# Performance work log

Hardware: AMD Instinct MI355X
Metric: run time of the kernel (lower is better)

Reference implementation:

```python
import jax, jax.numpy as jnp
import numpy as np

NUM_ITER = 3
SLOT_DIM = 16
INPUT_DIM = 256
HIDDEN_DIM = 128
EPS = 1e-8
LN_EPS = 1e-5  # torch LayerNorm default


def _layernorm(x, w, b):
    mu = jnp.mean(x, axis=-1, keepdims=True)
    var = jnp.mean((x - mu) ** 2, axis=-1, keepdims=True)
    return (x - mu) * jax.lax.rsqrt(var + LN_EPS) * w + b


def setup_inputs() -> dict:
    key = jax.random.key(0)
    ks = jax.random.split(key, 12)
    B, N, K = 32, 4096, 8
    D, S, H = INPUT_DIM, SLOT_DIM, HIDDEN_DIM
    inputs = jax.random.normal(ks[0], (B, N, D), dtype=jnp.float32)
    init_slots = jax.random.normal(ks[1], (B, K, S), dtype=jnp.float32)
    return {
        "inputs": inputs,
        "init_slots": init_slots,
        "ln_in_w": jnp.ones((D,), jnp.float32),
        "ln_in_b": jnp.zeros((D,), jnp.float32),
        "ln_s_w": jnp.ones((S,), jnp.float32),
        "ln_s_b": jnp.zeros((S,), jnp.float32),
        "ln_m_w": jnp.ones((S,), jnp.float32),
        "ln_m_b": jnp.zeros((S,), jnp.float32),
        "wq": jax.random.normal(ks[2], (S, S), jnp.float32) * (S ** -0.5),
        "wk": jax.random.normal(ks[3], (S, D), jnp.float32) * (D ** -0.5),
        "wv": jax.random.normal(ks[4], (S, D), jnp.float32) * (D ** -0.5),
        "w_ih": jax.random.normal(ks[5], (3 * S, S), jnp.float32) * (S ** -0.5),
        "w_hh": jax.random.normal(ks[6], (3 * S, S), jnp.float32) * (S ** -0.5),
        "b_ih": jnp.zeros((3 * S,), jnp.float32),
        "b_hh": jnp.zeros((3 * S,), jnp.float32),
        "mlp_w1": jax.random.normal(ks[7], (H, S), jnp.float32) * (S ** -0.5),
        "mlp_b1": jnp.zeros((H,), jnp.float32),
        "mlp_w2": jax.random.normal(ks[8], (S, H), jnp.float32) * (H ** -0.5),
        "mlp_b2": jnp.zeros((S,), jnp.float32),
    }


def _gru_cell(x, h, w_ih, w_hh, b_ih, b_hh):
    # torch GRUCell: gates ordered [r, z, n]
    gi = x @ w_ih.T + b_ih            # [BK, 3S]
    gh = h @ w_hh.T + b_hh
    i_r, i_z, i_n = jnp.split(gi, 3, axis=-1)
    h_r, h_z, h_n = jnp.split(gh, 3, axis=-1)
    r = jax.nn.sigmoid(i_r + h_r)
    z = jax.nn.sigmoid(i_z + h_z)
    n = jnp.tanh(i_n + r * h_n)
    return (1.0 - z) * n + z * h


def reference(inputs, init_slots, ln_in_w, ln_in_b, ln_s_w, ln_s_b, ln_m_w, ln_m_b,
              wq, wk, wv, w_ih, w_hh, b_ih, b_hh, mlp_w1, mlp_b1, mlp_w2, mlp_b2):
    B, N, _ = inputs.shape
    K = init_slots.shape[1]
    scale = SLOT_DIM ** -0.5

    x = _layernorm(inputs, ln_in_w, ln_in_b)
    k = jnp.einsum('bnd,sd->bns', x, wk)   # [B,N,S]
    v = jnp.einsum('bnd,sd->bns', x, wv)

    slots = init_slots
    attn = None
    for _ in range(NUM_ITER):
        slots_prev = slots
        q = jnp.einsum('bks,ts->bkt', _layernorm(slots, ln_s_w, ln_s_b), wq)
        logits = jnp.einsum('bks,bns->bkn', q, k) * scale       # [B,K,N]
        attn = jax.nn.softmax(logits, axis=1) + EPS              # softmax over SLOTS
        attn = attn / jnp.sum(attn, axis=-1, keepdims=True)
        updates = jnp.einsum('bkn,bns->bks', attn, v)            # [B,K,S]
        h = _gru_cell(updates.reshape(B * K, -1), slots_prev.reshape(B * K, -1),
                      w_ih, w_hh, b_ih, b_hh).reshape(B, K, -1)
        y = _layernorm(h, ln_m_w, ln_m_b)
        mlp = jax.nn.relu(y @ mlp_w1.T + mlp_b1) @ mlp_w2.T + mlp_b2
        slots = h + mlp
    return slots, attn
```

## Files before the change

### kernel.cpp

```cpp
#include <hip/hip_runtime.h>
#include <cstddef>


typedef unsigned short ushort_t;
typedef __attribute__((ext_vector_type(8))) short short8;
typedef __attribute__((ext_vector_type(4))) float f32x4;

__device__ __forceinline__ float sigmoid_f(float x){ return 1.f/(1.f+__expf(-x)); }
__device__ __forceinline__ float tanh_f(float x){ return 1.f - 2.f/(__expf(2.f*x)+1.f); }

__device__ __forceinline__ ushort_t f2bf(float x){
  unsigned u = __float_as_uint(x);
  return (ushort_t)((u + 0x7FFFu + ((u>>16)&1u)) >> 16);
}
__device__ __forceinline__ float bf2f(ushort_t b){
  return __uint_as_float(((unsigned)b) << 16);
}
__device__ __forceinline__ void split_bf(float v, short& hi, short& lo){
  unsigned u = __float_as_uint(v);
  hi = (short)(u >> 16);
  float hf = __uint_as_float(u & 0xFFFF0000u);
  lo = (short)(__float_as_uint(v - hf) >> 16);
}

__device__ __forceinline__ unsigned ld_cohpt(const unsigned* p){
  unsigned v;
  asm volatile("global_load_dword %0, %1, off sc0 sc1\n\t"
               "s_waitcnt vmcnt(0)"
               : "=v"(v) : "v"(p) : "memory");
  return v;
}

__global__ __launch_bounds__(256) void k_prep(
    const float* __restrict__ lnw, const float* __restrict__ lnb,
    const float* __restrict__ wk, const float* __restrict__ wv,
    const float* __restrict__ init_slots,
    const float* __restrict__ ln_s_w, const float* __restrict__ ln_s_b,
    const float* __restrict__ wq,
    ushort_t* __restrict__ Wh, ushort_t* __restrict__ Wl,
    float* __restrict__ mt,
    float* __restrict__ qbuf, float* __restrict__ upd, float* __restrict__ Abuf,
    unsigned* __restrict__ bar,
    float* __restrict__ slots_out)
{
  int t = threadIdx.x;
  int i = blockIdx.x*256 + t;
  {
    int s = i >> 8, d = i & 255;
    float w = (s < 16) ? wk[s*256+d] : wv[(s-16)*256+d];
    float w0 = lnw[d]*w;
    ushort_t hb = f2bf(w0);
    ushort_t lb = f2bf(w0 - bf2f(hb));
    Wh[i] = hb; Wl[i] = lb;
  }
  if (blockIdx.x != 0) return;
  {
    int s = t >> 3, j = t & 7;
    float m = 0.f, tv = 0.f;
    for (int d = j; d < 256; d += 8) {
      float w = (s < 16) ? wk[s*256+d] : wv[(s-16)*256+d];
      float w0 = lnw[d]*w;
      ushort_t hb = f2bf(w0);
      float hf = bf2f(hb);
      float lf = bf2f(f2bf(w0 - hf));
      m  += hf + lf;
      tv  = fmaf(lnb[d], w, tv);
    }
    m += __shfl_xor(m,1);  m += __shfl_xor(m,2);  m += __shfl_xor(m,4);
    tv += __shfl_xor(tv,1); tv += __shfl_xor(tv,2); tv += __shfl_xor(tv,4);
    if (j == 0) { mt[s] = m; mt[32+s] = tv; }
  }
  #pragma unroll
  for (int j2 = 0; j2 < 16; ++j2)
    slots_out[t*16+j2] = init_slots[t*16+j2];
  for (int i2 = t; i2 < 12288; i2 += 256) upd[i2] = 0.f;
  for (int i2 = t; i2 < 768;   i2 += 256) Abuf[i2] = 0.f;
  if (t < 96) bar[t] = 0u;
  float sl[16];
  #pragma unroll
  for (int j2 = 0; j2 < 16; ++j2) sl[j2] = init_slots[t*16+j2];
  float mu = 0.f;
  #pragma unroll
  for (int j2 = 0; j2 < 16; ++j2) mu += sl[j2];
  mu *= (1.f/16.f);
  float var = 0.f;
  #pragma unroll
  for (int j2 = 0; j2 < 16; ++j2) { float d = sl[j2]-mu; var = fmaf(d,d,var); }
  var *= (1.f/16.f);
  float rstd = rsqrtf(var + 1e-5f);
  float y[16];
  #pragma unroll
  for (int j2 = 0; j2 < 16; ++j2) y[j2] = (sl[j2]-mu)*rstd*ln_s_w[j2] + ln_s_b[j2];
  #pragma unroll
  for (int tq = 0; tq < 16; ++tq) {
    float q = 0.f;
    #pragma unroll
    for (int s2 = 0; s2 < 16; ++s2) q = fmaf(y[s2], wq[tq*16+s2], q);
    qbuf[t*16+tq] = q;
  }
}

#define VT_OFF    0
#define QS_OFF    16896
#define SLOTS_OFF 17408
#define APART_OFF 17920
#define X_OFF     18048
#define KLDS_OFF  (X_OFF + 33792)
#define PT_OFF    X_OFF
#define GW_OFF    (X_OFF + 8448)
#define SMEM_BYTES (X_OFF + 51200)

__global__ __launch_bounds__(256, 2) void k_mega(
    const float* __restrict__ x,
    const ushort_t* __restrict__ Wh, const ushort_t* __restrict__ Wl,
    const float* __restrict__ mt, const float* __restrict__ qbuf,
    const float* __restrict__ init_slots,
    float* __restrict__ upd, float* __restrict__ Abuf,
    unsigned* __restrict__ bar,
    float* __restrict__ slots_out, float* __restrict__ attn_out,
    const float* __restrict__ w_ih, const float* __restrict__ w_hh,
    const float* __restrict__ b_ih, const float* __restrict__ b_hh,
    const float* __restrict__ mlp_w1, const float* __restrict__ mlp_b1,
    const float* __restrict__ mlp_w2, const float* __restrict__ mlp_b2,
    const float* __restrict__ ln_m_w, const float* __restrict__ ln_m_b,
    const float* __restrict__ ln_s_w, const float* __restrict__ ln_s_b,
    const float* __restrict__ wq)
{
  __shared__ __align__(16) unsigned char smem[SMEM_BYTES];
  ushort_t* vt     = (ushort_t*)(smem + VT_OFF);
  float*    qs     = (float*)(smem + QS_OFF);
  float*    sslots = (float*)(smem + SLOTS_OFF);
  float*    apart  = (float*)(smem + APART_OFF);
  ushort_t* wlds   = (ushort_t*)(smem + X_OFF);
  float*    klds   = (float*)(smem + KLDS_OFF);
  ushort_t* pt     = (ushort_t*)(smem + PT_OFF);
  float*    s_wih  = (float*)(smem + GW_OFF);
  float*    s_whh  = s_wih + 48*17;
  float*    s_w1   = s_whh + 48*17;
  float*    s_w2   = s_w1 + 128*17;
  float*    s_bih  = s_w2 + 16*129;
  float*    s_bhh  = s_bih + 48;
  float*    s_b1   = s_bhh + 48;
  float*    s_b2   = s_b1 + 128;
  float*    s_lnmw = s_b2 + 16;
  float*    s_lnmb = s_lnmw + 16;
  float*    s_lnsw = s_lnmb + 16;
  float*    s_lnsb = s_lnsw + 16;
  float*    s_wq   = s_lnsb + 16;

  int t = threadIdx.x;
  int lane = t & 63;
  int w = t >> 6;
  int b  = blockIdx.x >> 4;
  int nc = blockIdx.x & 15;
  int n0 = nc << 8;

  {
    const unsigned* srcH = (const unsigned*)Wh;
    const unsigned* srcL = (const unsigned*)Wl;
    unsigned* dst = (unsigned*)wlds;
    #pragma unroll
    for (int i0 = 0; i0 < 8192; i0 += 256) {
      int i = i0 + t;
      int r = i >> 7, ww = i & 127;
      unsigned v = (r < 32) ? srcH[r*128 + ww] : srcL[(r-32)*128 + ww];
      dst[r*132 + ww] = v;
    }
  }
  __syncthreads();

  int m = lane & 15, quad = lane >> 4;
  const ushort_t* rhk = wlds + (size_t)m*264 + quad*8;
  const ushort_t* rhv = wlds + (size_t)(16+m)*264 + quad*8;
  const ushort_t* rlk = wlds + (size_t)(32+m)*264 + quad*8;
  const ushort_t* rlv = wlds + (size_t)(48+m)*264 + quad*8;
  float mtk  = mt[m],    mtv  = mt[16+m];
  float mtkb = mt[32+m], mtvb = mt[48+m];

  #pragma unroll
  for (int tile = 0; tile < 4; ++tile) {
    const float* xr = x + (size_t)(b*4096 + n0 + tile*64 + w*16 + m)*256 + quad*8;
    float4 xreg[16];
    #pragma unroll
    for (int kk = 0; kk < 8; ++kk) {
      xreg[2*kk]   = *(const float4*)(xr + kk*32);
      xreg[2*kk+1] = *(const float4*)(xr + kk*32 + 4);
    }
    f32x4 acck = {0.f,0.f,0.f,0.f}, accv = {0.f,0.f,0.f,0.f};
    float sum = 0.f, sumsq = 0.f;
    #pragma unroll
    for (int kk = 0; kk < 8; ++kk) {
      short8 bh_k = *(const short8*)(rhk + kk*32);
      short8 bh_v = *(const short8*)(rhv + kk*32);
      short8 bl_k = *(const short8*)(rlk + kk*32);
      short8 bl_v = *(const short8*)(rlv + kk*32);
      float xv[8] = {xreg[2*kk].x, xreg[2*kk].y, xreg[2*kk].z, xreg[2*kk].w,
                     xreg[2*kk+1].x, xreg[2*kk+1].y, xreg[2*kk+1].z, xreg[2*kk+1].w};
      short8 ah, al;
      #pragma unroll
      for (int j = 0; j < 8; ++j) {
        float v = xv[j];
        sum += v; sumsq = fmaf(v, v, sumsq);
        short h_, l_;
        split_bf(v, h_, l_);
        ah[j] = h_; al[j] = l_;
      }
      acck = __builtin_amdgcn_mfma_f32_16x16x32_bf16(ah, bh_k, acck, 0, 0, 0);
      accv = __builtin_amdgcn_mfma_f32_16x16x32_bf16(ah, bh_v, accv, 0, 0, 0);
      acck = __builtin_amdgcn_mfma_f32_16x16x32_bf16(al, bh_k, acck, 0, 0, 0);
      accv = __builtin_amdgcn_mfma_f32_16x16x32_bf16(al, bh_v, accv, 0, 0, 0);
      acck = __builtin_amdgcn_mfma_f32_16x16x32_bf16(ah, bl_k, acck, 0, 0, 0);
      accv = __builtin_amdgcn_mfma_f32_16x16x32_bf16(ah, bl_v, accv, 0, 0, 0);
    }
    sum   += __shfl_xor(sum, 16);   sum   += __shfl_xor(sum, 32);
    sumsq += __shfl_xor(sumsq, 16); sumsq += __shfl_xor(sumsq, 32);
    #pragma unroll
    for (int r = 0; r < 4; ++r) {
      int row = quad*4 + r;
      float s_ = __shfl(sum,   row);
      float q_ = __shfl(sumsq, row);
      float mu = s_*(1.f/256.f);
      float var = q_*(1.f/256.f) - mu*mu;
      float rstd = rsqrtf(var + 1e-5f);
      float ok = fmaf(rstd, acck[r] - mu*mtk, mtkb);
      float ov = fmaf(rstd, accv[r] - mu*mtv, mtvb);
      int gr = tile*64 + w*16 + row;
      klds[gr*17 + m] = ok;
      short h_, l_;
      split_bf(ov, h_, l_);
      vt[m*264 + gr]      = (ushort_t)h_;
      vt[(16+m)*264 + gr] = (ushort_t)l_;
    }
  }
  __syncthreads();
  float kv[16];
  #pragma unroll
  for (int j = 0; j < 16; ++j) kv[j] = klds[t*17 + j];
  __syncthreads();

  for (int i = t; i < 768; i += 256) {
    int g = i >> 4, j = i & 15;
    s_wih[g*17+j] = w_ih[i];
    s_whh[g*17+j] = w_hh[i];
  }
  for (int i = t; i < 2048; i += 256) {
    int r = i >> 4, c = i & 15;
    s_w1[r*17+c] = mlp_w1[i];
    int r2 = i >> 7, c2 = i & 127;
    s_w2[r2*129+c2] = mlp_w2[i];
  }
  if (t < 48) { s_bih[t] = b_ih[t]; s_bhh[t] = b_hh[t]; }
  if (t < 128) s_b1[t] = mlp_b1[t];
  if (t < 16) {
    s_b2[t] = mlp_b2[t];
    s_lnmw[t] = ln_m_w[t]; s_lnmb[t] = ln_m_b[t];
    s_lnsw[t] = ln_s_w[t]; s_lnsb[t] = ln_s_b[t];
  }
  for (int i = t; i < 256; i += 256) {
    int r = i >> 4, c = i & 15;
    s_wq[r*17+c] = wq[i];
  }
  if (t < 128) {
    qs[t]     = qbuf[b*128 + t];
    sslots[t] = init_slots[b*128 + t];
  }
  __syncthreads();

  const short8 z8 = {0,0,0,0,0,0,0,0};
  #pragma unroll 1
  for (int it = 0; it < 3; ++it) {
    float* upd_it = upd  + it*4096;
    float* Ab_it  = Abuf + it*256;

    float p8[8];
    {
      float lg[8];
      #pragma unroll
      for (int kk = 0; kk < 8; ++kk) {
        float a = 0.f;
        #pragma unroll
        for (int s = 0; s < 16; ++s) a = fmaf(qs[kk*16+s], kv[s], a);
        lg[kk] = a*0.25f;
      }
      float mx = lg[0];
      #pragma unroll
      for (int kk = 1; kk < 8; ++kk) mx = fmaxf(mx, lg[kk]);
      float se = 0.f;
      #pragma unroll
      for (int kk = 0; kk < 8; ++kk) { lg[kk] = __expf(lg[kk]-mx); se += lg[kk]; }
      float inv = 1.f/se;
      #pragma unroll
      for (int kk = 0; kk < 8; ++kk) p8[kk] = fmaf(lg[kk], inv, 1e-8f);
    }
    #pragma unroll
    for (int kk = 0; kk < 8; ++kk) {
      float r = p8[kk];
      r += __shfl_xor(r, 1);  r += __shfl_xor(r, 2);  r += __shfl_xor(r, 4);
      r += __shfl_xor(r, 8);  r += __shfl_xor(r, 16); r += __shfl_xor(r, 32);
      if (lane == 0) apart[w*8 + kk] = r;
    }
    #pragma unroll
    for (int kk = 0; kk < 8; ++kk) {
      short h_, l_;
      split_bf(p8[kk], h_, l_);
      pt[kk*264 + t]     = (ushort_t)h_;
      pt[(8+kk)*264 + t] = (ushort_t)l_;
    }
    __syncthreads();
    if (t < 8)
      atomicAdd(Ab_it + b*8 + t,
                apart[t] + apart[8+t] + apart[16+t] + apart[24+t]);
    if (w == 0) {
      int mm = lane & 15, q2 = lane >> 4;
      f32x4 acc = {0.f,0.f,0.f,0.f};
      #pragma unroll
      for (int c = 0; c < 8; ++c) {
        int k0 = c*32 + q2*8;
        short8 ah = (mm < 8) ? *(const short8*)&pt[mm*264 + k0]     : z8;
        short8 al = (mm < 8) ? *(const short8*)&pt[(8+mm)*264 + k0] : z8;
        short8 bh = *(const short8*)&vt[mm*264 + k0];
        short8 bl = *(const short8*)&vt[(16+mm)*264 + k0];
        acc = __builtin_amdgcn_mfma_f32_16x16x32_bf16(ah, bh, acc, 0, 0, 0);
        acc = __builtin_amdgcn_mfma_f32_16x16x32_bf16(al, bh, acc, 0, 0, 0);
        acc = __builtin_amdgcn_mfma_f32_16x16x32_bf16(ah, bl, acc, 0, 0, 0);
      }
      int s = lane & 15;
      #pragma unroll
      for (int r = 0; r < 4; ++r) {
        int kk = q2*4 + r;
        if (kk < 8) atomicAdd(upd_it + (b*8+kk)*16 + s, acc[r]);
      }
    }

    __syncthreads();
    if (t == 0) {
      unsigned* bp = bar + it*32 + b;
      asm volatile("s_waitcnt vmcnt(0)" ::: "memory");
      atomicAdd(bp, 1u);
      #pragma unroll 1
      for (int spin = 0; spin < (1<<18); ++spin) {
        if (ld_cohpt(bp) >= 16u) break;
        __builtin_amdgcn_s_sleep(2);
      }
    }
    __syncthreads();

    if (it == 2) {
      #pragma unroll
      for (int kk = 0; kk < 8; ++kk) {
        float Abk = __hip_atomic_load(Ab_it + b*8 + kk,
                                      __ATOMIC_RELAXED, __HIP_MEMORY_SCOPE_AGENT);
        attn_out[((size_t)(b*8 + kk))*4096 + n0 + t] = p8[kk]*(1.f/Abk);
      }
    }
    if (t < 128 && (it < 2 || nc == 0)) {
      int bk8 = t >> 4, s = t & 15;
      int laneBase = (t & 63) & ~15;
      float Ab = __hip_atomic_load(Ab_it + b*8 + bk8,
                                   __ATOMIC_RELAXED, __HIP_MEMORY_SCOPE_AGENT);
      float invA = 1.f / Ab;
      float u[16], h[16];
      #pragma unroll
      for (int j = 0; j < 16; ++j) {
        u[j] = __hip_atomic_load(upd_it + (b*8 + bk8)*16 + j,
                                 __ATOMIC_RELAXED, __HIP_MEMORY_SCOPE_AGENT) * invA;
        h[j] = sslots[bk8*16 + j];
      }
      float hs = h[s];
      float gir = s_bih[s],  giz = s_bih[16+s], gin = s_bih[32+s];
      float ghr = s_bhh[s],  ghz = s_bhh[16+s], ghn = s_bhh[32+s];
      #pragma unroll
      for (int j = 0; j < 16; ++j) {
        gir = fmaf(u[j], s_wih[s*17+j], gir);
        giz = fmaf(u[j], s_wih[(16+s)*17+j], giz);
        gin = fmaf(u[j], s_wih[(32+s)*17+j], gin);
        ghr = fmaf(h[j], s_whh[s*17+j], ghr);
        ghz = fmaf(h[j], s_whh[(16+s)*17+j], ghz);
        ghn = fmaf(h[j], s_whh[(32+s)*17+j], ghn);
      }
      float rr_ = sigmoid_f(gir + ghr);
      float zz = sigmoid_f(giz + ghz);
      float nn = tanh_f(gin + rr_*ghn);
      float hn = (1.f - zz)*nn + zz*hs;

      float ssum = hn;
      #pragma unroll
      for (int mm = 1; mm < 16; mm <<= 1) ssum += __shfl_xor(ssum, mm);
      float mu = ssum*(1.f/16.f);
      float dv = hn - mu;
      float vs = dv*dv;
      #pragma unroll
      for (int mm = 1; mm < 16; mm <<= 1) vs += __shfl_xor(vs, mm);
      float rstd = rsqrtf(vs*(1.f/16.f) + 1e-5f);
      float y = dv*rstd*s_lnmw[s] + s_lnmb[s];

      float yv[16];
      #pragma unroll
      for (int j = 0; j < 16; ++j) yv[j] = __shfl(y, laneBase + j);

      float h1[8];
      #pragma unroll
      for (int i = 0; i < 8; ++i) {
        int jj = i*16 + s;
        float a = s_b1[jj];
        #pragma unroll
        for (int q = 0; q < 16; ++q) a = fmaf(yv[q], s_w1[jj*17+q], a);
        h1[i] = fmaxf(a, 0.f);
      }
      float o = s_b2[s];
      #pragma unroll
      for (int i = 0; i < 8; ++i) {
        #pragma unroll
        for (int sp = 0; sp < 16; ++sp) {
          float hv = __shfl(h1[i], laneBase + sp);
          o = fmaf(hv, s_w2[s*129 + i*16 + sp], o);
        }
      }
      float slot_new = hn + o;
      if (it < 2) {
        sslots[bk8*16 + s] = slot_new;
        float ss = slot_new;
        #pragma unroll
        for (int mm = 1; mm < 16; mm <<= 1) ss += __shfl_xor(ss, mm);
        float mu2 = ss*(1.f/16.f);
        float d2 = slot_new - mu2;
        float v2 = d2*d2;
        #pragma unroll
        for (int mm = 1; mm < 16; mm <<= 1) v2 += __shfl_xor(v2, mm);
        float rstd2 = rsqrtf(v2*(1.f/16.f) + 1e-5f);
        float y2 = d2*rstd2*s_lnsw[s] + s_lnsb[s];
        float qv = 0.f;
        #pragma unroll
        for (int sp = 0; sp < 16; ++sp)
          qv = fmaf(__shfl(y2, laneBase + sp), s_wq[s*17+sp], qv);
        qs[bk8*16 + s] = qv;
      } else {
        slots_out[(b*8 + bk8)*16 + s] = slot_new;
      }
    }
    __syncthreads();
  }
}


__global__ __launch_bounds__(256, 4) void k_proj(
    const float* __restrict__ x, const ushort_t* __restrict__ Wh,
    const ushort_t* __restrict__ Wl, const float* __restrict__ mt,
    float* __restrict__ kout, float* __restrict__ vout)
{
  __shared__ ushort_t wlds[64*264];
  int t = threadIdx.x;
  int lane = t & 63;
  int p = __builtin_amdgcn_readfirstlane(t >> 6);
  int m = lane & 15, quad = lane >> 4;
  int r0 = blockIdx.x*64;
  {
    const unsigned* srcH = (const unsigned*)Wh;
    const unsigned* srcL = (const unsigned*)Wl;
    unsigned* dst = (unsigned*)wlds;
    #pragma unroll
    for (int i0 = 0; i0 < 8192; i0 += 256) {
      int i = i0 + t;
      int r = i >> 7, w = i & 127;
      unsigned v = (r < 32) ? srcH[r*128 + w] : srcL[(r-32)*128 + w];
      dst[r*132 + w] = v;
    }
  }
  __syncthreads();

  const ushort_t* rhk = wlds + (size_t)m*264 + quad*8;
  const ushort_t* rhv = wlds + (size_t)(16+m)*264 + quad*8;
  const ushort_t* rlk = wlds + (size_t)(32+m)*264 + quad*8;
  const ushort_t* rlv = wlds + (size_t)(48+m)*264 + quad*8;

  const float* xr = x + (size_t)(r0 + p*16 + m)*256 + quad*8;

  f32x4 acck = {0.f,0.f,0.f,0.f}, accv = {0.f,0.f,0.f,0.f};
  float sum = 0.f, sumsq = 0.f;

  #pragma unroll
  for (int kk = 0; kk < 8; ++kk) {
    float4 a0 = *(const float4*)(xr + kk*32);
    float4 a1 = *(const float4*)(xr + kk*32 + 4);
    short8 bh_k = *(const short8*)(rhk + kk*32);
    short8 bh_v = *(const short8*)(rhv + kk*32);
    short8 bl_k = *(const short8*)(rlk + kk*32);
    short8 bl_v = *(const short8*)(rlv + kk*32);
    float xv[8] = {a0.x,a0.y,a0.z,a0.w, a1.x,a1.y,a1.z,a1.w};
    short8 ah, al;
    #pragma unroll
    for (int j = 0; j < 8; ++j) {
      float v = xv[j];
      sum += v; sumsq = fmaf(v, v, sumsq);
      short h_, l_;
      split_bf(v, h_, l_);
      ah[j] = h_; al[j] = l_;
    }
    acck = __builtin_amdgcn_mfma_f32_16x16x32_bf16(ah, bh_k, acck, 0, 0, 0);
    accv = __builtin_amdgcn_mfma_f32_16x16x32_bf16(ah, bh_v, accv, 0, 0, 0);
    acck = __builtin_amdgcn_mfma_f32_16x16x32_bf16(al, bh_k, acck, 0, 0, 0);
    accv = __builtin_amdgcn_mfma_f32_16x16x32_bf16(al, bh_v, accv, 0, 0, 0);
    acck = __builtin_amdgcn_mfma_f32_16x16x32_bf16(ah, bl_k, acck, 0, 0, 0);
    accv = __builtin_amdgcn_mfma_f32_16x16x32_bf16(ah, bl_v, accv, 0, 0, 0);
  }

  sum   += __shfl_xor(sum, 16);  sum   += __shfl_xor(sum, 32);
  sumsq += __shfl_xor(sumsq, 16); sumsq += __shfl_xor(sumsq, 32);

  float mtk  = mt[m],    mtv  = mt[16+m];
  float mtkb = mt[32+m], mtvb = mt[48+m];
  #pragma unroll
  for (int r = 0; r < 4; ++r) {
    int row = quad*4 + r;
    float s_ = __shfl(sum,   row);
    float q_ = __shfl(sumsq, row);
    float mu = s_*(1.f/256.f);
    float var = q_*(1.f/256.f) - mu*mu;
    float rstd = rsqrtf(var + 1e-5f);
    float ok = fmaf(rstd, acck[r] - mu*mtk, mtkb);
    float ov = fmaf(rstd, accv[r] - mu*mtv, mtvb);
    size_t grow = (size_t)(r0 + p*16 + row)*16 + m;
    kout[grow] = ok;
    vout[grow] = ov;
  }
}

__global__ __launch_bounds__(256) void k_attn(
    const float* __restrict__ kproj, const float* __restrict__ vproj,
    const float* __restrict__ qbuf,
    float* __restrict__ upd, float* __restrict__ Abuf,
    float* __restrict__ attn_out, int write_attn)
{
  __shared__ ushort_t vt[32*264];
  __shared__ ushort_t pt[32*264];
  __shared__ float qs[128];
  __shared__ float apart[4][8];
  int b = blockIdx.x >> 4;
  int n0 = (blockIdx.x & 15) * 256;
  int t = threadIdx.x;
  int w = t >> 6, lane = t & 63;

  if (t < 128) qs[t] = qbuf[b*128 + t];

  const float* kr = kproj + ((size_t)(b*4096 + n0 + t))*16;
  const float* vr = vproj + ((size_t)(b*4096 + n0 + t))*16;
  float kv[16], vv[16];
  #pragma unroll
  for (int j = 0; j < 16; j += 4) {
    float4 f = *(const float4*)(kr+j);
    kv[j]=f.x; kv[j+1]=f.y; kv[j+2]=f.z; kv[j+3]=f.w;
    float4 g = *(const float4*)(vr+j);
    vv[j]=g.x; vv[j+1]=g.y; vv[j+2]=g.z; vv[j+3]=g.w;
  }
  #pragma unroll
  for (int s = 0; s < 16; ++s) {
    short h_, l_;
    split_bf(vv[s], h_, l_);
    vt[s*264 + t] = (ushort_t)h_;
    vt[(16+s)*264 + t] = (ushort_t)l_;
  }
  __syncthreads();

  float p8[8];
  {
    float lg[8];
    #pragma unroll
    for (int kk = 0; kk < 8; ++kk) {
      float a = 0.f;
      #pragma unroll
      for (int s = 0; s < 16; ++s) a = fmaf(qs[kk*16+s], kv[s], a);
      lg[kk] = a*0.25f;
    }
    float mx = lg[0];
    #pragma unroll
    for (int kk = 1; kk < 8; ++kk) mx = fmaxf(mx, lg[kk]);
    float se = 0.f;
    #pragma unroll
    for (int kk = 0; kk < 8; ++kk) { lg[kk] = __expf(lg[kk]-mx); se += lg[kk]; }
    float inv = 1.f/se;
    #pragma unroll
    for (int kk = 0; kk < 8; ++kk) {
      float pv = fmaf(lg[kk], inv, 1e-8f);
      p8[kk] = pv;
      if (write_attn) attn_out[((size_t)(b*8+kk))*4096 + n0 + t] = pv;
    }
  }
  #pragma unroll
  for (int kk = 0; kk < 8; ++kk) {
    float r = p8[kk];
    r += __shfl_xor(r, 1);  r += __shfl_xor(r, 2);  r += __shfl_xor(r, 4);
    r += __shfl_xor(r, 8);  r += __shfl_xor(r, 16); r += __shfl_xor(r, 32);
    if (lane == 0) apart[w][kk] = r;
  }
  #pragma unroll
  for (int kk = 0; kk < 8; ++kk) {
    short h_, l_;
    split_bf(p8[kk], h_, l_);
    pt[kk*264 + t] = (ushort_t)h_;
    pt[(16+kk)*264 + t] = (ushort_t)l_;
  }
  __syncthreads();

  if (t < 8)
    atomicAdd(Abuf + b*8 + t,
              apart[0][t] + apart[1][t] + apart[2][t] + apart[3][t]);

  if (w == 0) {
    int mm = lane & 15, quad = lane >> 4;
    const short8 z8 = {0,0,0,0,0,0,0,0};
    f32x4 acc = {0.f,0.f,0.f,0.f};
    #pragma unroll
    for (int c = 0; c < 8; ++c) {
      int k0 = c*32 + quad*8;
      short8 ah = (mm < 8) ? *(const short8*)&pt[mm*264 + k0]      : z8;
      short8 al = (mm < 8) ? *(const short8*)&pt[(16+mm)*264 + k0] : z8;
      short8 bh = *(const short8*)&vt[mm*264 + k0];
      short8 bl = *(const short8*)&vt[(16+mm)*264 + k0];
      acc = __builtin_amdgcn_mfma_f32_16x16x32_bf16(ah, bh, acc, 0, 0, 0);
      acc = __builtin_amdgcn_mfma_f32_16x16x32_bf16(al, bh, acc, 0, 0, 0);
      acc = __builtin_amdgcn_mfma_f32_16x16x32_bf16(ah, bl, acc, 0, 0, 0);
    }
    int s = lane & 15;
    #pragma unroll
    for (int r = 0; r < 4; ++r) {
      int kk = quad*4 + r;
      if (kk < 8) atomicAdd(upd + (b*8+kk)*16 + s, acc[r]);
    }
  }
}

__device__ __forceinline__ void gru_body(
    int bk, int s, int laneBase, int prep_next,
    float* upd, float* Abuf, float* slots, float* qbuf,
    const float* s_wih, const float* s_whh,
    const float* s_bih, const float* s_bhh,
    const float* s_w1, const float* s_b1,
    const float* s_w2, const float* s_b2,
    const float* s_lnmw, const float* s_lnmb,
    const float* s_lnsw, const float* s_lnsb, const float* s_wq)
{
  float inv = 1.f / Abuf[bk];
  float u[16], h[16];
  #pragma unroll
  for (int j = 0; j < 16; ++j) {
    u[j] = upd[bk*16+j] * inv;
    h[j] = slots[bk*16+j];
  }
  float hs = slots[bk*16+s];

  float gir = s_bih[s],  giz = s_bih[16+s], gin = s_bih[32+s];
  float ghr = s_bhh[s],  ghz = s_bhh[16+s], ghn = s_bhh[32+s];
  #pragma unroll
  for (int j = 0; j < 16; ++j) {
    gir = fmaf(u[j], s_wih[s*17+j], gir);
    giz = fmaf(u[j], s_wih[(16+s)*17+j], giz);
    gin = fmaf(u[j], s_wih[(32+s)*17+j], gin);
    ghr = fmaf(h[j], s_whh[s*17+j], ghr);
    ghz = fmaf(h[j], s_whh[(16+s)*17+j], ghz);
    ghn = fmaf(h[j], s_whh[(32+s)*17+j], ghn);
  }
  float rr = sigmoid_f(gir + ghr);
  float zz = sigmoid_f(giz + ghz);
  float nn = tanh_f(gin + rr*ghn);
  float hn = (1.f-zz)*nn + zz*hs;

  float ssum = hn;
  #pragma unroll
  for (int mm = 1; mm < 16; mm <<= 1) ssum += __shfl_xor(ssum, mm);
  float mu = ssum*(1.f/16.f);
  float dv = hn - mu;
  float vs = dv*dv;
  #pragma unroll
  for (int mm = 1; mm < 16; mm <<= 1) vs += __shfl_xor(vs, mm);
  float rstd = rsqrtf(vs*(1.f/16.f) + 1e-5f);
  float y = dv*rstd*s_lnmw[s] + s_lnmb[s];

  float yv[16];
  #pragma unroll
  for (int j = 0; j < 16; ++j) yv[j] = __shfl(y, laneBase + j);

  float h1[8];
  #pragma unroll
  for (int i = 0; i < 8; ++i) {
    int jj = i*16 + s;
    float a = s_b1[jj];
    #pragma unroll
    for (int q = 0; q < 16; ++q) a = fmaf(yv[q], s_w1[jj*17+q], a);
    h1[i] = fmaxf(a, 0.f);
  }
  float o = s_b2[s];
  #pragma unroll
  for (int i = 0; i < 8; ++i) {
    #pragma unroll
    for (int sp = 0; sp < 16; ++sp) {
      float hv = __shfl(h1[i], laneBase + sp);
      o = fmaf(hv, s_w2[s*129 + i*16 + sp], o);
    }
  }
  float slot_new = hn + o;
  slots[bk*16+s] = slot_new;

  if (prep_next) {
    float ss = slot_new;
    #pragma unroll
    for (int mm = 1; mm < 16; mm <<= 1) ss += __shfl_xor(ss, mm);
    float mu2 = ss*(1.f/16.f);
    float d2 = slot_new - mu2;
    float v2 = d2*d2;
    #pragma unroll
    for (int mm = 1; mm < 16; mm <<= 1) v2 += __shfl_xor(v2, mm);
    float rstd2 = rsqrtf(v2*(1.f/16.f) + 1e-5f);
    float y2 = d2*rstd2*s_lnsw[s] + s_lnsb[s];
    float qv = 0.f;
    #pragma unroll
    for (int sp = 0; sp < 16; ++sp)
      qv = fmaf(__shfl(y2, laneBase+sp), s_wq[s*17+sp], qv);
    qbuf[bk*16+s] = qv;
    upd[bk*16+s] = 0.f;
    if (s == 0) Abuf[bk] = 0.f;
  }
}

#define GRU_STAGE_LDS()                                                      \
  __shared__ float s_wih[48*17], s_whh[48*17];                               \
  __shared__ float s_bih[48], s_bhh[48];                                     \
  __shared__ float s_w1[128*17], s_b1[128];                                  \
  __shared__ float s_w2[16*129], s_b2[16];                                   \
  __shared__ float s_lnmw[16], s_lnmb[16], s_lnsw[16], s_lnsb[16];           \
  __shared__ float s_wq[16*17];                                              \
  {                                                                          \
    int t_ = threadIdx.x;                                                    \
    for (int i = t_; i < 768; i += 256) {                                    \
      int g = i >> 4, j = i & 15;                                            \
      s_wih[g*17+j] = w_ih[i];                                               \
      s_whh[g*17+j] = w_hh[i];                                               \
    }                                                                        \
    for (int i = t_; i < 2048; i += 256) {                                   \
      int r = i >> 4, c = i & 15;                                            \
      s_w1[r*17+c] = mlp_w1[i];                                              \
      int r2 = i >> 7, c2 = i & 127;                                         \
      s_w2[r2*129+c2] = mlp_w2[i];                                           \
    }                                                                        \
    if (t_ < 48) { s_bih[t_] = b_ih[t_]; s_bhh[t_] = b_hh[t_]; }             \
    if (t_ < 128) s_b1[t_] = mlp_b1[t_];                                     \
    if (t_ < 16) {                                                           \
      s_b2[t_] = mlp_b2[t_];                                                 \
      s_lnmw[t_] = ln_m_w[t_]; s_lnmb[t_] = ln_m_b[t_];                      \
      s_lnsw[t_] = ln_s_w[t_]; s_lnsb[t_] = ln_s_b[t_];                      \
    }                                                                        \
    for (int i = t_; i < 256; i += 256) {                                    \
      int r = i >> 4, c = i & 15;                                            \
      s_wq[r*17+c] = wq[i];                                                  \
    }                                                                        \
  }                                                                          \
  __syncthreads();

__global__ __launch_bounds__(256) void k_gru(
    float* __restrict__ upd, float* __restrict__ Abuf,
    float* __restrict__ slots, float* __restrict__ qbuf,
    const float* __restrict__ w_ih, const float* __restrict__ w_hh,
    const float* __restrict__ b_ih, const float* __restrict__ b_hh,
    const float* __restrict__ mlp_w1, const float* __restrict__ mlp_b1,
    const float* __restrict__ mlp_w2, const float* __restrict__ mlp_b2,
    const float* __restrict__ ln_m_w, const float* __restrict__ ln_m_b,
    const float* __restrict__ ln_s_w, const float* __restrict__ ln_s_b,
    const float* __restrict__ wq)
{
  GRU_STAGE_LDS()
  int t = threadIdx.x;
  int bk = blockIdx.x*16 + (t >> 4);
  int s = t & 15;
  int laneBase = (t & 63) & ~15;
  gru_body(bk, s, laneBase, 1, upd, Abuf, slots, qbuf,
           s_wih, s_whh, s_bih, s_bhh, s_w1, s_b1, s_w2, s_b2,
           s_lnmw, s_lnmb, s_lnsw, s_lnsb, s_wq);
}

__global__ __launch_bounds__(256) void k_final(
    float* __restrict__ upd, float* __restrict__ Abuf,
    float* __restrict__ slots, float* __restrict__ qbuf,
    float* __restrict__ attn,
    const float* __restrict__ w_ih, const float* __restrict__ w_hh,
    const float* __restrict__ b_ih, const float* __restrict__ b_hh,
    const float* __restrict__ mlp_w1, const float* __restrict__ mlp_b1,
    const float* __restrict__ mlp_w2, const float* __restrict__ mlp_b2,
    const float* __restrict__ ln_m_w, const float* __restrict__ ln_m_b,
    const float* __restrict__ ln_s_w, const float* __restrict__ ln_s_b,
    const float* __restrict__ wq)
{
  int t = threadIdx.x;
  {
    int bk = blockIdx.x;
    float inv = 1.f / Abuf[bk];
    float4* p = (float4*)(attn + (size_t)bk*4096);
    #pragma unroll 4
    for (int i = t; i < 1024; i += 256) {
      float4 v = p[i];
      v.x *= inv; v.y *= inv; v.z *= inv; v.w *= inv;
      p[i] = v;
    }
  }
  if (blockIdx.x >= 16) return;
  GRU_STAGE_LDS()
  int bk = blockIdx.x*16 + (t >> 4);
  int s = t & 15;
  int laneBase = (t & 63) & ~15;
  gru_body(bk, s, laneBase, 0, upd, Abuf, slots, qbuf,
           s_wih, s_whh, s_bih, s_bhh, s_w1, s_b1, s_w2, s_b2,
           s_lnmw, s_lnmb, s_lnsw, s_lnsb, s_wq);
}

extern "C" void kernel_launch(void* const* d_in, const int* in_sizes, int n_in,
                              void* d_out, int out_size, void* d_ws, size_t ws_size,
                              hipStream_t stream)
{
  const float* inputs     = (const float*)d_in[0];
  const float* init_slots = (const float*)d_in[1];
  const float* ln_in_w    = (const float*)d_in[2];
  const float* ln_in_b    = (const float*)d_in[3];
  const float* ln_s_w     = (const float*)d_in[4];
  const float* ln_s_b     = (const float*)d_in[5];
  const float* ln_m_w     = (const float*)d_in[6];
  const float* ln_m_b     = (const float*)d_in[7];
  const float* wq         = (const float*)d_in[8];
  const float* wk         = (const float*)d_in[9];
  const float* wv         = (const float*)d_in[10];
  const float* w_ih       = (const float*)d_in[11];
  const float* w_hh       = (const float*)d_in[12];
  const float* b_ih       = (const float*)d_in[13];
  const float* b_hh       = (const float*)d_in[14];
  const float* mlp_w1     = (const float*)d_in[15];
  const float* mlp_b1     = (const float*)d_in[16];
  const float* mlp_w2     = (const float*)d_in[17];
  const float* mlp_b2     = (const float*)d_in[18];

  float* ws    = (float*)d_ws;
  ushort_t* Wh = (ushort_t*)ws;
  ushort_t* Wl = (ushort_t*)(ws + 4096);
  float* mt    = ws + 8192;
  float* qbuf  = ws + 8320;
  float* upd   = ws + 12416;
  float* Abuf  = ws + 24704;
  unsigned* bar = (unsigned*)(ws + 25472);
  float* kproj = ws + 25600;
  float* vproj = kproj + 2097152;

  float* out   = (float*)d_out;
  float* slots = out;
  float* attn  = out + 4096;

  static int s_mode = -1;
  if (s_mode < 0) {
    int dev = 0;
    (void)hipGetDevice(&dev);
    int ncu = 0;
    (void)hipDeviceGetAttribute(&ncu, hipDeviceAttributeMultiprocessorCount, dev);
    int nb = 0;
    if (hipOccupancyMaxActiveBlocksPerMultiprocessor(&nb, (const void*)k_mega,
                                                     256, 0) != hipSuccess)
      nb = 0;
    s_mode = (nb > 0 && ncu > 0 && (long)nb * ncu >= 512) ? 0 : 1;
  }

  k_prep<<<32, 256, 0, stream>>>(ln_in_w, ln_in_b, wk, wv, init_slots,
                                 ln_s_w, ln_s_b, wq,
                                 Wh, Wl, mt, qbuf, upd, Abuf, bar, slots);

  if (s_mode == 0) {
    k_mega<<<512, 256, 0, stream>>>(inputs, Wh, Wl, mt, qbuf, init_slots,
                                    upd, Abuf, bar, slots, attn,
                                    w_ih, w_hh, b_ih, b_hh,
                                    mlp_w1, mlp_b1, mlp_w2, mlp_b2,
                                    ln_m_w, ln_m_b, ln_s_w, ln_s_b, wq);
    return;
  }

  {
    void* kargs[] = {
      (void*)&inputs, (void*)&Wh, (void*)&Wl, (void*)&mt, (void*)&qbuf,
      (void*)&init_slots, (void*)&upd, (void*)&Abuf, (void*)&bar,
      (void*)&slots, (void*)&attn, (void*)&w_ih, (void*)&w_hh,
      (void*)&b_ih, (void*)&b_hh, (void*)&mlp_w1, (void*)&mlp_b1,
      (void*)&mlp_w2, (void*)&mlp_b2, (void*)&ln_m_w, (void*)&ln_m_b,
      (void*)&ln_s_w, (void*)&ln_s_b, (void*)&wq };
    hipError_t err = hipLaunchCooperativeKernel((const void*)k_mega,
                                                dim3(512), dim3(256),
                                                kargs, 0, stream);
    if (err == hipSuccess) return;
    (void)hipGetLastError();
  }

  k_proj<<<2048, 256, 0, stream>>>(inputs, Wh, Wl, mt, kproj, vproj);
  for (int it = 0; it < 3; ++it) {
    int last = (it == 2);
    k_attn<<<512, 256, 0, stream>>>(kproj, vproj, qbuf, upd, Abuf, attn, last);
    if (!last)
      k_gru<<<16, 256, 0, stream>>>(upd, Abuf, slots, qbuf,
                                    w_ih, w_hh, b_ih, b_hh,
                                    mlp_w1, mlp_b1, mlp_w2, mlp_b2,
                                    ln_m_w, ln_m_b, ln_s_w, ln_s_b, wq);
  }
  k_final<<<256, 256, 0, stream>>>(upd, Abuf, slots, qbuf, attn,
                                   w_ih, w_hh, b_ih, b_hh,
                                   mlp_w1, mlp_b1, mlp_w2, mlp_b2,
                                   ln_m_w, ln_m_b, ln_s_w, ln_s_b, wq);
}
```

Before: 335.5 us.

## Fold prep into mega kernel and replace atomics with per-chunk partial buffers

```diff
diff --git a/kernel.cpp b/kernel.cpp
--- a/kernel.cpp
+++ b/kernel.cpp
@@ -30,81 +30,20 @@
                : "=v"(v) : "v"(p) : "memory");
   return v;
 }
-
-__global__ __launch_bounds__(256) void k_prep(
-    const float* __restrict__ lnw, const float* __restrict__ lnb,
-    const float* __restrict__ wk, const float* __restrict__ wv,
-    const float* __restrict__ init_slots,
-    const float* __restrict__ ln_s_w, const float* __restrict__ ln_s_b,
-    const float* __restrict__ wq,
-    ushort_t* __restrict__ Wh, ushort_t* __restrict__ Wl,
-    float* __restrict__ mt,
-    float* __restrict__ qbuf, float* __restrict__ upd, float* __restrict__ Abuf,
-    unsigned* __restrict__ bar,
-    float* __restrict__ slots_out)
-{
-  int t = threadIdx.x;
-  int i = blockIdx.x*256 + t;
-  {
-    int s = i >> 8, d = i & 255;
-    float w = (s < 16) ? wk[s*256+d] : wv[(s-16)*256+d];
-    float w0 = lnw[d]*w;
-    ushort_t hb = f2bf(w0);
-    ushort_t lb = f2bf(w0 - bf2f(hb));
-    Wh[i] = hb; Wl[i] = lb;
-  }
-  if (blockIdx.x != 0) return;
-  {
-    int s = t >> 3, j = t & 7;
-    float m = 0.f, tv = 0.f;
-    for (int d = j; d < 256; d += 8) {
-      float w = (s < 16) ? wk[s*256+d] : wv[(s-16)*256+d];
-      float w0 = lnw[d]*w;
-      ushort_t hb = f2bf(w0);
-      float hf = bf2f(hb);
-      float lf = bf2f(f2bf(w0 - hf));
-      m  += hf + lf;
-      tv  = fmaf(lnb[d], w, tv);
-    }
-    m += __shfl_xor(m,1);  m += __shfl_xor(m,2);  m += __shfl_xor(m,4);
-    tv += __shfl_xor(tv,1); tv += __shfl_xor(tv,2); tv += __shfl_xor(tv,4);
-    if (j == 0) { mt[s] = m; mt[32+s] = tv; }
-  }
-  #pragma unroll
-  for (int j2 = 0; j2 < 16; ++j2)
-    slots_out[t*16+j2] = init_slots[t*16+j2];
-  for (int i2 = t; i2 < 12288; i2 += 256) upd[i2] = 0.f;
-  for (int i2 = t; i2 < 768;   i2 += 256) Abuf[i2] = 0.f;
-  if (t < 96) bar[t] = 0u;
-  float sl[16];
-  #pragma unroll
-  for (int j2 = 0; j2 < 16; ++j2) sl[j2] = init_slots[t*16+j2];
-  float mu = 0.f;
-  #pragma unroll
-  for (int j2 = 0; j2 < 16; ++j2) mu += sl[j2];
-  mu *= (1.f/16.f);
-  float var = 0.f;
-  #pragma unroll
-  for (int j2 = 0; j2 < 16; ++j2) { float d = sl[j2]-mu; var = fmaf(d,d,var); }
-  var *= (1.f/16.f);
-  float rstd = rsqrtf(var + 1e-5f);
-  float y[16];
-  #pragma unroll
-  for (int j2 = 0; j2 < 16; ++j2) y[j2] = (sl[j2]-mu)*rstd*ln_s_w[j2] + ln_s_b[j2];
-  #pragma unroll
-  for (int tq = 0; tq < 16; ++tq) {
-    float q = 0.f;
-    #pragma unroll
-    for (int s2 = 0; s2 < 16; ++s2) q = fmaf(y[s2], wq[tq*16+s2], q);
-    qbuf[t*16+tq] = q;
-  }
+__device__ __forceinline__ void st_agent(float* p, float v){
+  __hip_atomic_store(p, v, __ATOMIC_RELAXED, __HIP_MEMORY_SCOPE_AGENT);
+}
+__device__ __forceinline__ float ld_agent(const float* p){
+  return __hip_atomic_load(p, __ATOMIC_RELAXED, __HIP_MEMORY_SCOPE_AGENT);
 }
 
 #define VT_OFF    0
 #define QS_OFF    16896
 #define SLOTS_OFF 17408
 #define APART_OFF 17920
-#define X_OFF     18048
+#define ULDS_OFF  18048
+#define MT_OFF    18560
+#define X_OFF     18816
 #define KLDS_OFF  (X_OFF + 33792)
 #define PT_OFF    X_OFF
 #define GW_OFF    (X_OFF + 8448)
@@ -112,11 +51,11 @@
 
 __global__ __launch_bounds__(256, 2) void k_mega(
     const float* __restrict__ x,
-    const ushort_t* __restrict__ Wh, const ushort_t* __restrict__ Wl,
-    const float* __restrict__ mt, const float* __restrict__ qbuf,
+    const float* __restrict__ wk, const float* __restrict__ wv,
+    const float* __restrict__ lnw, const float* __restrict__ lnb,
     const float* __restrict__ init_slots,
-    float* __restrict__ upd, float* __restrict__ Abuf,
-    unsigned* __restrict__ bar,
+    float* __restrict__ updp, float* __restrict__ Asum,
+    unsigned* __restrict__ barp,
     float* __restrict__ slots_out, float* __restrict__ attn_out,
     const float* __restrict__ w_ih, const float* __restrict__ w_hh,
     const float* __restrict__ b_ih, const float* __restrict__ b_hh,
@@ -131,6 +70,8 @@
   float*    qs     = (float*)(smem + QS_OFF);
   float*    sslots = (float*)(smem + SLOTS_OFF);
   float*    apart  = (float*)(smem + APART_OFF);
+  float*    ulds   = (float*)(smem + ULDS_OFF);
+  float*    mtf    = (float*)(smem + MT_OFF);
   ushort_t* wlds   = (ushort_t*)(smem + X_OFF);
   float*    klds   = (float*)(smem + KLDS_OFF);
   ushort_t* pt     = (ushort_t*)(smem + PT_OFF);
@@ -156,17 +97,69 @@
   int n0 = nc << 8;
 
   {
-    const unsigned* srcH = (const unsigned*)Wh;
-    const unsigned* srcL = (const unsigned*)Wl;
     unsigned* dst = (unsigned*)wlds;
     #pragma unroll
     for (int i0 = 0; i0 < 8192; i0 += 256) {
       int i = i0 + t;
       int r = i >> 7, ww = i & 127;
-      unsigned v = (r < 32) ? srcH[r*128 + ww] : srcL[(r-32)*128 + ww];
-      dst[r*132 + ww] = v;
-    }
-  }
+      int s = (r & 31);
+      int d = ww*2;
+      float wa = (s < 16) ? wk[s*256+d]   : wv[(s-16)*256+d];
+      float wb = (s < 16) ? wk[s*256+d+1] : wv[(s-16)*256+d+1];
+      float w0a = lnw[d]*wa, w0b = lnw[d+1]*wb;
+      ushort_t ha = f2bf(w0a), hb2 = f2bf(w0b);
+      unsigned word;
+      if (r < 32) {
+        word = (unsigned)ha | ((unsigned)hb2 << 16);
+      } else {
+        ushort_t la = f2bf(w0a - bf2f(ha));
+        ushort_t lb = f2bf(w0b - bf2f(hb2));
+        word = (unsigned)la | ((unsigned)lb << 16);
+      }
+      dst[r*132 + ww] = word;
+    }
+  }
+  {
+    int s = t >> 3, j = t & 7;
+    float m = 0.f, tv = 0.f;
+    for (int d = j; d < 256; d += 8) {
+      float w_ = (s < 16) ? wk[s*256+d] : wv[(s-16)*256+d];
+      float w0 = lnw[d]*w_;
+      ushort_t hb = f2bf(w0);
+      float hf = bf2f(hb);
+      float lf = bf2f(f2bf(w0 - hf));
+      m  += hf + lf;
+      tv  = fmaf(lnb[d], w_, tv);
+    }
+    m += __shfl_xor(m,1);  m += __shfl_xor(m,2);  m += __shfl_xor(m,4);
+    tv += __shfl_xor(tv,1); tv += __shfl_xor(tv,2); tv += __shfl_xor(tv,4);
+    if (j == 0) { mtf[s] = m; mtf[32+s] = tv; }
+  }
+  if (t < 8) {
+    float sl[16];
+    #pragma unroll
+    for (int j2 = 0; j2 < 16; ++j2) sl[j2] = init_slots[(b*8+t)*16+j2];
+    float mu = 0.f;
+    #pragma unroll
+    for (int j2 = 0; j2 < 16; ++j2) mu += sl[j2];
+    mu *= (1.f/16.f);
+    float var = 0.f;
+    #pragma unroll
+    for (int j2 = 0; j2 < 16; ++j2) { float d = sl[j2]-mu; var = fmaf(d,d,var); }
+    var *= (1.f/16.f);
+    float rstd = rsqrtf(var + 1e-5f);
+    float y[16];
+    #pragma unroll
+    for (int j2 = 0; j2 < 16; ++j2) y[j2] = (sl[j2]-mu)*rstd*ln_s_w[j2] + ln_s_b[j2];
+    #pragma unroll
+    for (int tq = 0; tq < 16; ++tq) {
+      float q = 0.f;
+      #pragma unroll
+      for (int s2 = 0; s2 < 16; ++s2) q = fmaf(y[s2], wq[tq*16+s2], q);
+      qs[t*16+tq] = q;
+    }
+  }
+  if (t < 128) sslots[t] = init_slots[b*128 + t];
   __syncthreads();
 
   int m = lane & 15, quad = lane >> 4;
@@ -174,8 +167,8 @@
   const ushort_t* rhv = wlds + (size_t)(16+m)*264 + quad*8;
   const ushort_t* rlk = wlds + (size_t)(32+m)*264 + quad*8;
   const ushort_t* rlv = wlds + (size_t)(48+m)*264 + quad*8;
-  float mtk  = mt[m],    mtv  = mt[16+m];
-  float mtkb = mt[32+m], mtvb = mt[48+m];
+  float mtk  = mtf[m],    mtv  = mtf[16+m];
+  float mtkb = mtf[32+m], mtvb = mtf[48+m];
 
   #pragma unroll
   for (int tile = 0; tile < 4; ++tile) {
@@ -260,17 +253,13 @@
     int r = i >> 4, c = i & 15;
     s_wq[r*17+c] = wq[i];
   }
-  if (t < 128) {
-    qs[t]     = qbuf[b*128 + t];
-    sslots[t] = init_slots[b*128 + t];
-  }
   __syncthreads();
 
   const short8 z8 = {0,0,0,0,0,0,0,0};
   #pragma unroll 1
   for (int it = 0; it < 3; ++it) {
-    float* upd_it = upd  + it*4096;
-    float* Ab_it  = Abuf + it*256;
+    float* upd_it = updp + (size_t)(it*32 + b)*2048;
+    float* As_it  = Asum + (size_t)(it*32 + b)*128;
 
     float p8[8];
     {
@@ -308,8 +297,8 @@
     }
     __syncthreads();
     if (t < 8)
-      atomicAdd(Ab_it + b*8 + t,
-                apart[t] + apart[8+t] + apart[16+t] + apart[24+t]);
+      st_agent(As_it + nc*8 + t,
+               apart[t] + apart[8+t] + apart[16+t] + apart[24+t]);
     if (w == 0) {
       int mm = lane & 15, q2 = lane >> 4;
       f32x4 acc = {0.f,0.f,0.f,0.f};
@@ -328,42 +317,52 @@
       #pragma unroll
       for (int r = 0; r < 4; ++r) {
         int kk = q2*4 + r;
-        if (kk < 8) atomicAdd(upd_it + (b*8+kk)*16 + s, acc[r]);
+        if (kk < 8) st_agent(upd_it + nc*128 + kk*16 + s, acc[r]);
       }
     }
 
     __syncthreads();
     if (t == 0) {
-      unsigned* bp = bar + it*32 + b;
+      unsigned* bp = barp + (it*32 + b)*32;
       asm volatile("s_waitcnt vmcnt(0)" ::: "memory");
       atomicAdd(bp, 1u);
       #pragma unroll 1
       for (int spin = 0; spin < (1<<18); ++spin) {
         if (ld_cohpt(bp) >= 16u) break;
-        __builtin_amdgcn_s_sleep(2);
+        __builtin_amdgcn_s_sleep(8);
       }
     }
     __syncthreads();
 
+    if (t < 8) {
+      float a = 0.f;
+      #pragma unroll
+      for (int nc2 = 0; nc2 < 16; ++nc2) a += ld_agent(As_it + nc2*8 + t);
+      apart[t] = a;
+    }
+    if (t < 128) {
+      int bk8 = t >> 4, s = t & 15;
+      float us = 0.f;
+      #pragma unroll
+      for (int nc2 = 0; nc2 < 16; ++nc2)
+        us += ld_agent(upd_it + nc2*128 + bk8*16 + s);
+      ulds[t] = us;
+    }
+    __syncthreads();
+
     if (it == 2) {
       #pragma unroll
-      for (int kk = 0; kk < 8; ++kk) {
-        float Abk = __hip_atomic_load(Ab_it + b*8 + kk,
-                                      __ATOMIC_RELAXED, __HIP_MEMORY_SCOPE_AGENT);
-        attn_out[((size_t)(b*8 + kk))*4096 + n0 + t] = p8[kk]*(1.f/Abk);
-      }
+      for (int kk = 0; kk < 8; ++kk)
+        attn_out[((size_t)(b*8 + kk))*4096 + n0 + t] = p8[kk]*(1.f/apart[kk]);
     }
     if (t < 128 && (it < 2 || nc == 0)) {
       int bk8 = t >> 4, s = t & 15;
       int laneBase = (t & 63) & ~15;
-      float Ab = __hip_atomic_load(Ab_it + b*8 + bk8,
-                                   __ATOMIC_RELAXED, __HIP_MEMORY_SCOPE_AGENT);
-      float invA = 1.f / Ab;
+      float invA = 1.f / apart[bk8];
       float u[16], h[16];
       #pragma unroll
       for (int j = 0; j < 16; ++j) {
-        u[j] = __hip_atomic_load(upd_it + (b*8 + bk8)*16 + j,
-                                 __ATOMIC_RELAXED, __HIP_MEMORY_SCOPE_AGENT) * invA;
+        u[j] = ulds[bk8*16 + j] * invA;
         h[j] = sslots[bk8*16 + j];
       }
       float hs = h[s];
@@ -442,6 +441,74 @@
   }
 }
 
+
+__global__ __launch_bounds__(256) void k_prep(
+    const float* __restrict__ lnw, const float* __restrict__ lnb,
+    const float* __restrict__ wk, const float* __restrict__ wv,
+    const float* __restrict__ init_slots,
+    const float* __restrict__ ln_s_w, const float* __restrict__ ln_s_b,
+    const float* __restrict__ wq,
+    ushort_t* __restrict__ Wh, ushort_t* __restrict__ Wl,
+    float* __restrict__ mt,
+    float* __restrict__ qbuf, float* __restrict__ upd, float* __restrict__ Abuf,
+    float* __restrict__ slots_out)
+{
+  int t = threadIdx.x;
+  int i = blockIdx.x*256 + t;
+  {
+    int s = i >> 8, d = i & 255;
+    float w = (s < 16) ? wk[s*256+d] : wv[(s-16)*256+d];
+    float w0 = lnw[d]*w;
+    ushort_t hb = f2bf(w0);
+    ushort_t lb = f2bf(w0 - bf2f(hb));
+    Wh[i] = hb; Wl[i] = lb;
+  }
+  if (blockIdx.x != 0) return;
+  {
+    int s = t >> 3, j = t & 7;
+    float m = 0.f, tv = 0.f;
+    for (int d = j; d < 256; d += 8) {
+      float w = (s < 16) ? wk[s*256+d] : wv[(s-16)*256+d];
+      float w0 = lnw[d]*w;
+      ushort_t hb = f2bf(w0);
+      float hf = bf2f(hb);
+      float lf = bf2f(f2bf(w0 - hf));
+      m  += hf + lf;
+      tv  = fmaf(lnb[d], w, tv);
+    }
+    m += __shfl_xor(m,1);  m += __shfl_xor(m,2);  m += __shfl_xor(m,4);
+    tv += __shfl_xor(tv,1); tv += __shfl_xor(tv,2); tv += __shfl_xor(tv,4);
+    if (j == 0) { mt[s] = m; mt[32+s] = tv; }
+  }
+  #pragma unroll
+  for (int j2 = 0; j2 < 16; ++j2) {
+    slots_out[t*16+j2] = init_slots[t*16+j2];
+    upd[t*16+j2] = 0.f;
+  }
+  Abuf[t] = 0.f;
+  float sl[16];
+  #pragma unroll
+  for (int j2 = 0; j2 < 16; ++j2) sl[j2] = init_slots[t*16+j2];
+  float mu = 0.f;
+  #pragma unroll
+  for (int j2 = 0; j2 < 16; ++j2) mu += sl[j2];
+  mu *= (1.f/16.f);
+  float var = 0.f;
+  #pragma unroll
+  for (int j2 = 0; j2 < 16; ++j2) { float d = sl[j2]-mu; var = fmaf(d,d,var); }
+  var *= (1.f/16.f);
+  float rstd = rsqrtf(var + 1e-5f);
+  float y[16];
+  #pragma unroll
+  for (int j2 = 0; j2 < 16; ++j2) y[j2] = (sl[j2]-mu)*rstd*ln_s_w[j2] + ln_s_b[j2];
+  #pragma unroll
+  for (int tq = 0; tq < 16; ++tq) {
+    float q = 0.f;
+    #pragma unroll
+    for (int s2 = 0; s2 < 16; ++s2) q = fmaf(y[s2], wq[tq*16+s2], q);
+    qbuf[t*16+tq] = q;
+  }
+}
 
 __global__ __launch_bounds__(256, 4) void k_proj(
     const float* __restrict__ x, const ushort_t* __restrict__ Wh,
@@ -834,15 +901,18 @@
   const float* mlp_w2     = (const float*)d_in[17];
   const float* mlp_b2     = (const float*)d_in[18];
 
-  float* ws    = (float*)d_ws;
-  ushort_t* Wh = (ushort_t*)ws;
-  ushort_t* Wl = (ushort_t*)(ws + 4096);
-  float* mt    = ws + 8192;
-  float* qbuf  = ws + 8320;
-  float* upd   = ws + 12416;
-  float* Abuf  = ws + 24704;
-  unsigned* bar = (unsigned*)(ws + 25472);
-  float* kproj = ws + 25600;
+  float* ws = (float*)d_ws;
+  unsigned* barp = (unsigned*)ws;
+  float* updp = ws + 3072;
+  float* Asum = ws + 3072 + 196608;
+  float* lg    = ws + 211968;
+  ushort_t* Wh = (ushort_t*)lg;
+  ushort_t* Wl = (ushort_t*)(lg + 4096);
+  float* mt    = lg + 8192;
+  float* qbuf  = lg + 8320;
+  float* upd   = lg + 12416;
+  float* Abuf  = lg + 16512;
+  float* kproj = lg + 16768;
   float* vproj = kproj + 2097152;
 
   float* out   = (float*)d_out;
@@ -862,13 +932,10 @@
     s_mode = (nb > 0 && ncu > 0 && (long)nb * ncu >= 512) ? 0 : 1;
   }
 
-  k_prep<<<32, 256, 0, stream>>>(ln_in_w, ln_in_b, wk, wv, init_slots,
-                                 ln_s_w, ln_s_b, wq,
-                                 Wh, Wl, mt, qbuf, upd, Abuf, bar, slots);
-
   if (s_mode == 0) {
-    k_mega<<<512, 256, 0, stream>>>(inputs, Wh, Wl, mt, qbuf, init_slots,
-                                    upd, Abuf, bar, slots, attn,
+    (void)hipMemsetAsync(barp, 0, 3*32*32*sizeof(unsigned), stream);
+    k_mega<<<512, 256, 0, stream>>>(inputs, wk, wv, ln_in_w, ln_in_b,
+                                    init_slots, updp, Asum, barp, slots, attn,
                                     w_ih, w_hh, b_ih, b_hh,
                                     mlp_w1, mlp_b1, mlp_w2, mlp_b2,
                                     ln_m_w, ln_m_b, ln_s_w, ln_s_b, wq);
@@ -876,9 +943,10 @@
   }
 
   {
+    (void)hipMemsetAsync(barp, 0, 3*32*32*sizeof(unsigned), stream);
     void* kargs[] = {
-      (void*)&inputs, (void*)&Wh, (void*)&Wl, (void*)&mt, (void*)&qbuf,
-      (void*)&init_slots, (void*)&upd, (void*)&Abuf, (void*)&bar,
+      (void*)&inputs, (void*)&wk, (void*)&wv, (void*)&ln_in_w, (void*)&ln_in_b,
+      (void*)&init_slots, (void*)&updp, (void*)&Asum, (void*)&barp,
       (void*)&slots, (void*)&attn, (void*)&w_ih, (void*)&w_hh,
       (void*)&b_ih, (void*)&b_hh, (void*)&mlp_w1, (void*)&mlp_b1,
       (void*)&mlp_w2, (void*)&mlp_b2, (void*)&ln_m_w, (void*)&ln_m_b,
@@ -890,6 +958,9 @@
     (void)hipGetLastError();
   }
 
+  k_prep<<<32, 256, 0, stream>>>(ln_in_w, ln_in_b, wk, wv, init_slots,
+                                 ln_s_w, ln_s_b, wq,
+                                 Wh, Wl, mt, qbuf, upd, Abuf, slots);
   k_proj<<<2048, 256, 0, stream>>>(inputs, Wh, Wl, mt, kproj, vproj);
   for (int it = 0; it < 3; ++it) {
     int last = (it == 2);
```

Measured after the change: 307.9 us. 1.09x faster.
